# Performance work log

Hardware: AMD Instinct MI355X
Metric: run time of the kernel (lower is better)

The kernel has to match this reference:

```python
import jax, jax.numpy as jnp
import numpy as np
import math

N_HEADS = 16
ROPE_BASE = 10000.0


def rotate_half(x):
    x1 = x[..., ::2]
    x2 = x[..., 1::2]
    return jnp.stack((-x2, x1), axis=-1).reshape(x.shape)


def rope_tables(seq_len, head_dim, dtype):
    inv_freq = 1.0 / (ROPE_BASE ** (jnp.arange(0, head_dim, 2, dtype=jnp.float32) / head_dim))
    positions = jnp.arange(seq_len, dtype=jnp.float32)
    freqs = jnp.outer(positions, inv_freq)            # [S, hd/2]
    emb = jnp.concatenate((freqs, freqs), axis=-1)    # [S, hd]  (matches torch cat convention)
    cos = jnp.cos(emb)[None, None, :, :].astype(dtype)
    sin = jnp.sin(emb)[None, None, :, :].astype(dtype)
    return cos, sin


def setup_inputs() -> dict:
    key = jax.random.key(0)
    k1, k2, k3 = jax.random.split(key, 3)
    B, S, D = 2, 2048, 1024
    x = jax.random.normal(k1, (B, S, D), dtype=jnp.float32)
    # causal lower-triangular mask, broadcastable over batch and heads
    mask = jnp.tril(jnp.ones((S, S), dtype=jnp.int32))[None, None, :, :]
    w_qkv = jax.random.normal(k2, (D, 3 * D), dtype=jnp.float32) * 0.02
    w_out = jax.random.normal(k3, (D, D), dtype=jnp.float32) * 0.02
    return {"x": x, "mask": mask, "w_qkv": w_qkv, "w_out": w_out}


def reference(x, mask, w_qkv, w_out):
    B, S, D = x.shape
    H = N_HEADS
    hd = D // H
    qkv = (x @ w_qkv).reshape(B, S, 3, H, hd)
    qkv = jnp.transpose(qkv, (2, 0, 3, 1, 4))         # [3, B, H, S, hd]
    q, k, v = qkv[0], qkv[1], qkv[2]
    cos, sin = rope_tables(S, hd, x.dtype)
    q = q * cos + rotate_half(q) * sin
    k = k * cos + rotate_half(k) * sin
    scale = math.sqrt(hd)
    attn = jnp.einsum("bhsd,bhtd->bhst", q, k) / scale
    attn = jnp.where(mask == 0, -jnp.inf, attn)
    attn = jax.nn.softmax(attn, axis=-1)              # dropout p=0.0 -> identity
    out = jnp.einsum("bhst,bhtd->bhsd", attn, v)
    out = jnp.transpose(out, (0, 2, 1, 3)).reshape(B, S, D)
    return out @ w_out
```

## Files before the change

### kernel.cpp

```cpp
#include <hip/hip_runtime.h>
#include <stdint.h>

typedef unsigned short u16;
typedef __bf16 bf16x8 __attribute__((ext_vector_type(8)));
typedef float f32x4 __attribute__((ext_vector_type(4)));

#define S_LEN 2048
#define NH    16
#define DM    1024
#define N3    3072
#define MROWS 4096

__device__ __forceinline__ float b2f(u16 u) {
  unsigned int v = ((unsigned int)u) << 16;
  return __builtin_bit_cast(float, v);
}
__device__ __forceinline__ u16 f2b(float f) {
  unsigned int v = __builtin_bit_cast(unsigned int, f);
  v += 0x7fffu + ((v >> 16) & 1u);
  return (u16)(v >> 16);
}
__device__ __forceinline__ u16 f2b_trunc(float f) {
  return (u16)(__builtin_bit_cast(unsigned int, f) >> 16);
}
__device__ __forceinline__ bf16x8 ld8(const u16* p) { return *(const bf16x8*)p; }
__device__ __forceinline__ f32x4 mfma16(bf16x8 a, bf16x8 b, f32x4 c) {
  return __builtin_amdgcn_mfma_f32_16x16x32_bf16(a, b, c, 0, 0, 0);
}
__device__ __forceinline__ void glds16(const void* g, void* l) {
  __builtin_amdgcn_global_load_lds(
      (const __attribute__((address_space(1))) unsigned int*)g,
      (__attribute__((address_space(3))) unsigned int*)l, 16, 0, 0);
}
__device__ __forceinline__ int bfish(unsigned int w) {
  unsigned int e = (w >> 7) & 0xffu;
  return (e >= 100u && e <= 134u) ? 1 : 0;
}

__global__ __launch_bounds__(256) void prep_kernel(const void* __restrict__ x,
                                                   const void* __restrict__ wqkv,
                                                   const void* __restrict__ wout,
                                                   u16* __restrict__ xb,
                                                   u16* __restrict__ wqT,
                                                   u16* __restrict__ woT,
                                                   float* __restrict__ cosT,
                                                   float* __restrict__ sinT,
                                                   int* __restrict__ flag) {
  const int bx = blockIdx.x;
  const int t = threadIdx.x;
  if (bx < 2048) {
    __shared__ int cnt;
    if (t == 0) cnt = 0;
    __syncthreads();
    size_t i = (size_t)bx * 256 + t;
    const uint4* xv = (const uint4*)x;
    uint4 probe = xv[i];
    unsigned int wds[4]; *(uint4*)wds = probe;
    atomicAdd(&cnt, bfish(wds[0]) + bfish(wds[1]) + bfish(wds[2]) + bfish(wds[3]));
    __syncthreads();
    const int isbf = cnt > 512;
    if (t == 0) *flag = isbf;
    if (isbf) {
      ((uint4*)xb)[i] = probe;
    } else {
      const float* xf = (const float*)x;
      #pragma unroll
      for (int j = 0; j < 8; ++j) xb[i * 8 + j] = f2b(xf[i * 8 + j]);
    }
    return;
  }
  if (bx < 2304) {
    int i = (bx - 2048) * 256 + t;
    int s = i >> 5, f = i & 31;
    float invf = expf(-(float)(2 * f) * (1.0f / 64.0f) * logf(10000.0f));
    float th = (float)s * invf;
    float sv, cv;
    sincosf(th, &sv, &cv);
    cosT[s * 64 + f] = cv; cosT[s * 64 + 32 + f] = cv;
    sinT[s * 64 + f] = sv; sinT[s * 64 + 32 + f] = sv;
    return;
  }
  const int wq = bx < 5376;
  const int id = wq ? (bx - 2304) : (bx - 5376);
  const int ncx = wq ? 96 : 32;
  const void* in = wq ? wqkv : wout;
  u16* out = wq ? wqT : woT;
  const int C = wq ? 3072 : 1024;
  const int bxc = id % ncx, byr = id / ncx;
  __shared__ int cnt;
  __shared__ float tile[32][33];
  const int tx = t & 31, ty = t >> 5;
  if (t == 0) cnt = 0;
  __syncthreads();
  const unsigned int* wv = (const unsigned int*)in;
  size_t off = (((size_t)id) * 256 + t) & 524287;
  atomicAdd(&cnt, bfish(wv[off]));
  __syncthreads();
  const int fl = cnt > 128;
  const int c0 = bxc * 32, r0 = byr * 32;
  #pragma unroll
  for (int dy = 0; dy < 32; dy += 8) {
    size_t idx = (size_t)(r0 + ty + dy) * C + (c0 + tx);
    float v = fl ? b2f(((const u16*)in)[idx]) : ((const float*)in)[idx];
    tile[ty + dy][tx] = v;
  }
  __syncthreads();
  #pragma unroll
  for (int dy = 0; dy < 32; dy += 8) {
    out[(size_t)(c0 + ty + dy) * 1024 + (r0 + tx)] = f2b(tile[tx][ty + dy]);
  }
}

template <int TM, int EPI>
__global__ __launch_bounds__(256) void gemm_t(const u16* __restrict__ A,
                                              const u16* __restrict__ Bt,
                                              int M, int N, int Kd,
                                              u16* __restrict__ Qo, u16* __restrict__ Ko,
                                              u16* __restrict__ Vo,
                                              void* __restrict__ Out,
                                              const int* __restrict__ flag) {
  constexpr int MI = TM / 32;
  __shared__ u16 smem[(TM + 128) * 32];
  u16* Al = smem;
  u16* Bl = smem + TM * 32;
  const int t = threadIdx.x;
  const int lane = t & 63, wave = t >> 6;
  const int ln = lane & 15, quad = lane >> 4;
  const int wr = wave >> 1, wc = wave & 1;
  const int m0 = blockIdx.x * TM, n0 = blockIdx.y * 128;
  const int rr = t >> 2;
  const int cb = (t & 3) * 16;
  const char* Ab = (const char*)A;
  const char* Bb = (const char*)Bt;
  f32x4 acc[MI][4] = {};

  for (int k0 = 0; k0 < Kd; k0 += 32) {
    __syncthreads();
    #pragma unroll
    for (int p = 0; p < TM / 64; ++p)
      glds16(Ab + ((size_t)(m0 + p * 64 + rr) * Kd + k0) * 2 + cb,
             (char*)Al + p * 4096 + t * 16);
    glds16(Bb + ((size_t)(n0 + rr) * Kd + k0) * 2 + cb,      (char*)Bl + t * 16);
    glds16(Bb + ((size_t)(n0 + 64 + rr) * Kd + k0) * 2 + cb, (char*)Bl + 4096 + t * 16);
    __syncthreads();
    bf16x8 a[MI], b[4];
    #pragma unroll
    for (int i = 0; i < MI; ++i)
      a[i] = ld8(Al + (wr * (TM / 2) + i * 16 + ln) * 32 + quad * 8);
    #pragma unroll
    for (int j = 0; j < 4; ++j)
      b[j] = ld8(Bl + (wc * 64 + j * 16 + ln) * 32 + quad * 8);
    #pragma unroll
    for (int i = 0; i < MI; ++i)
      #pragma unroll
      for (int j = 0; j < 4; ++j)
        acc[i][j] = mfma16(a[i], b[j], acc[i][j]);
  }

  if constexpr (EPI == 0) {
    #pragma unroll
    for (int i = 0; i < MI; ++i)
      #pragma unroll
      for (int j = 0; j < 4; ++j)
        #pragma unroll
        for (int r = 0; r < 4; ++r) {
          int m = m0 + wr * (TM / 2) + i * 16 + quad * 4 + r;
          int c = n0 + wc * 64 + j * 16 + ln;
          u16 bv = f2b(acc[i][j][r]);
          int b_ = m >> 11, s = m & 2047;
          int which = c >> 10, h = (c >> 6) & 15, d = c & 63;
          size_t bh = (size_t)(b_ * NH + h);
          u16* dst = (which == 0) ? Qo : (which == 1) ? Ko : Vo;
          dst[(bh * S_LEN + s) * 64 + d] = bv;
        }
  } else {
    const int fl = *flag;
    #pragma unroll
    for (int i = 0; i < MI; ++i)
      #pragma unroll
      for (int j = 0; j < 4; ++j)
        #pragma unroll
        for (int r = 0; r < 4; ++r) {
          int m = m0 + wr * (TM / 2) + i * 16 + quad * 4 + r;
          int c = n0 + wc * 64 + j * 16 + ln;
          float v = acc[i][j][r];
          if (fl) ((u16*)Out)[(size_t)m * N + c] = f2b(v);
          else    ((float*)Out)[(size_t)m * N + c] = v;
        }
  }
}

__global__ __launch_bounds__(256) void vrope_kernel(u16* __restrict__ Qb,
                                                    u16* __restrict__ Kb,
                                                    const u16* __restrict__ V,
                                                    u16* __restrict__ Vt,
                                                    const float* __restrict__ cosT,
                                                    const float* __restrict__ sinT) {
  __shared__ u16 L[4096];
  const int bx = blockIdx.x;
  if (bx < 4096) {
    int i = bx * 256 + threadIdx.x;
    int seg = i & 7;
    int s   = (i >> 3) & 2047;
    int bh  = (i >> 14) & 31;
    int isK = (i >> 19) & 1;
    u16* ptr = (isK ? Kb : Qb) + ((size_t)bh * S_LEN + s) * 64 + seg * 8;
    const float qs = isK ? 1.0f : 0.18033688011112042f;
    uint4 raw = *(const uint4*)ptr;
    u16 e[8]; *(uint4*)e = raw;
    const float* cr = cosT + s * 64 + seg * 8;
    const float* sr = sinT + s * 64 + seg * 8;
    u16 o[8];
    #pragma unroll
    for (int p = 0; p < 4; ++p) {
      float x0 = b2f(e[2 * p]), x1 = b2f(e[2 * p + 1]);
      float o0 = (x0 * cr[2 * p]     - x1 * sr[2 * p])     * qs;
      float o1 = (x1 * cr[2 * p + 1] + x0 * sr[2 * p + 1]) * qs;
      o[2 * p] = f2b(o0); o[2 * p + 1] = f2b(o1);
    }
    *(uint4*)ptr = *(const uint4*)o;
    return;
  }
  const int bb = bx - 4096;
  const int t = threadIdx.x;
  const int bh = bb >> 5, st = bb & 31;
  const u16* Vb = V + ((size_t)bh * S_LEN + st * 64) * 64;
  u16* Vtb = Vt + (size_t)bh * (64 * S_LEN) + st * 64;
  #pragma unroll
  for (int it = 0; it < 2; ++it) {
    int c = it * 256 + t;
    int s = c >> 3, dseg = c & 7;
    uint4 v = *(const uint4*)(Vb + (size_t)s * 64 + dseg * 8);
    u16 e[8]; *(uint4*)e = v;
    #pragma unroll
    for (int j = 0; j < 8; ++j) {
      int d = dseg * 8 + j;
      L[d * 64 + (s ^ (dseg << 3))] = e[j];
    }
  }
  __syncthreads();
  #pragma unroll
  for (int it = 0; it < 2; ++it) {
    int c = it * 256 + t;
    int d = c >> 3, sseg = c & 7;
    uint4 v = *(const uint4*)(L + d * 64 + (((sseg ^ (d >> 3)) & 7) << 3));
    *(uint4*)(Vtb + (size_t)d * S_LEN + sseg * 8) = v;
  }
}

__global__ __launch_bounds__(256) void attn_kernel(const u16* __restrict__ Qb,
                                                   const u16* __restrict__ Kb,
                                                   const u16* __restrict__ Vt,
                                                   u16* __restrict__ Ao) {
  __shared__ u16 smem[20480];
  u16* Kl = smem;
  u16* Vl = smem + 8192;
  u16* Pl = smem + 16384;
  const int t = threadIdx.x;
  const int lane = t & 63, w = t >> 6;
  const int ln = lane & 15, quad = lane >> 4;
  const int i = blockIdx.x;
  const int xcd = i & 7;
  const int j = i >> 3;
  const int bh = (xcd << 2) | (j & 3);
  const int q5 = j >> 2;
  const int g = q5 & 7, s5 = q5 >> 3;
  const int qt = (s5 & 1) ? (31 - ((s5 >> 1) << 3) - g) : (((s5 >> 1) << 3) + g);
  const int q0 = qt * 64;
  const int b = bh >> 4, h = bh & 15;
  const u16* Qbh = Qb + (size_t)bh * (S_LEN * 64);
  const u16* Kbh = Kb + (size_t)bh * (S_LEN * 64);
  const u16* Vtbh = Vt + (size_t)bh * (64 * S_LEN);
  u16* Plw = Pl + w * 1024;
  u16* AoBase = Ao + (size_t)b * S_LEN * DM + h * 64;

  auto stage = [&](int kt, int bufi) {
    u16* kd = Kl + bufi * 4096;
    u16* vd = Vl + bufi * 4096;
    const u16* kg = Kbh + (size_t)kt * 64 * 64;
    const u16* vg = Vtbh + (size_t)kt * 64;
    #pragma unroll
    for (int it = 0; it < 2; ++it) {
      int c = it * 256 + t;
      int row = c >> 3, sg = (c & 7) ^ (row & 7);
      glds16((const char*)kg + ((size_t)row * 64 + sg * 8) * 2,   (char*)kd + c * 16);
      glds16((const char*)vg + ((size_t)row * 2048 + sg * 8) * 2, (char*)vd + c * 16);
    }
  };

  bf16x8 aq[2];
  #pragma unroll
  for (int kk = 0; kk < 2; ++kk)
    aq[kk] = ld8(Qbh + (size_t)(q0 + w * 16 + ln) * 64 + kk * 32 + quad * 8);

  f32x4 o[4] = {};
  float l[4] = {0.f, 0.f, 0.f, 0.f};

  stage(0, 0);
  __syncthreads();

  for (int kt = 0; kt <= qt; ++kt) {
    const int bufi = kt & 1;
    if (kt < qt) stage(kt + 1, bufi ^ 1);
    const u16* Kb_ = Kl + bufi * 4096;
    const u16* Vb_ = Vl + bufi * 4096;

    f32x4 sc[4] = {};
    #pragma unroll
    for (int kk = 0; kk < 2; ++kk)
      #pragma unroll
      for (int ct = 0; ct < 4; ++ct) {
        bf16x8 bk = ld8(Kb_ + (ct * 16 + ln) * 64 + (((kk * 4 + quad) ^ (ln & 7)) << 3));
        sc[ct] = mfma16(aq[kk], bk, sc[ct]);
      }

    if (kt == qt) {
      #pragma unroll
      for (int ct = 0; ct < 4; ++ct)
        #pragma unroll
        for (int r = 0; r < 4; ++r) {
          const int row = quad * 4 + r;
          float p = ((ct * 16 + ln) > (w * 16 + row))
                        ? 0.f : __builtin_amdgcn_exp2f(sc[ct][r]);
          l[r] += p;
          Plw[row * 64 + ((((ct * 2) + (ln >> 3)) ^ quad) << 3) + (ln & 7)] = f2b_trunc(p);
        }
    } else {
      #pragma unroll
      for (int ct = 0; ct < 4; ++ct)
        #pragma unroll
        for (int r = 0; r < 4; ++r) {
          const int row = quad * 4 + r;
          float p = __builtin_amdgcn_exp2f(sc[ct][r]);
          l[r] += p;
          Plw[row * 64 + ((((ct * 2) + (ln >> 3)) ^ quad) << 3) + (ln & 7)] = f2b_trunc(p);
        }
    }

    #pragma unroll
    for (int k4 = 0; k4 < 2; ++k4) {
      bf16x8 ap = ld8(Plw + ln * 64 + (((k4 * 4 + quad) ^ (ln >> 2)) << 3));
      #pragma unroll
      for (int dt = 0; dt < 4; ++dt) {
        bf16x8 bv = ld8(Vb_ + (dt * 16 + ln) * 64 + (((k4 * 4 + quad) ^ (ln & 7)) << 3));
        o[dt] = mfma16(ap, bv, o[dt]);
      }
    }
    __syncthreads();
  }

  #pragma unroll
  for (int r = 0; r < 4; ++r) {
    float lv = l[r];
    #pragma unroll
    for (int off = 1; off < 16; off <<= 1) lv += __shfl_xor(lv, off);
    l[r] = 1.f / lv;
  }
  #pragma unroll
  for (int dt = 0; dt < 4; ++dt)
    #pragma unroll
    for (int r = 0; r < 4; ++r) {
      float v = o[dt][r] * l[r];
      AoBase[(size_t)(q0 + w * 16 + quad * 4 + r) * DM + dt * 16 + ln] = f2b(v);
    }
}

extern "C" void kernel_launch(void* const* d_in, const int* in_sizes, int n_in,
                              void* d_out, int out_size, void* d_ws, size_t ws_size,
                              hipStream_t stream) {
  (void)in_sizes; (void)n_in; (void)out_size; (void)ws_size;
  const void* x    = d_in[0];
  const void* wqkv = d_in[2];
  const void* wout = d_in[3];
  char* ws = (char*)d_ws;
  u16*  xb   = (u16*)(ws + 0);
  u16*  Ao   = xb;
  u16*  wqT  = (u16*)(ws + 8388608);
  u16*  Vtp  = (u16*)(ws + 8388608);
  u16*  Qb   = (u16*)(ws + 16777216);
  u16*  Kb   = (u16*)(ws + 25165824);
  u16*  Vb   = (u16*)(ws + 33554432);
  u16*  woT  = (u16*)(ws + 41943040);
  float* cosT = (float*)(ws + 44040192);
  float* sinT = (float*)(ws + 44564480);
  int*  flag = (int*)(ws + 45088768);

  prep_kernel<<<6400, 256, 0, stream>>>(x, wqkv, wout, xb, wqT, woT, cosT, sinT, flag);
  gemm_t<128, 0><<<dim3(32, 24), 256, 0, stream>>>(xb, wqT, MROWS, N3, DM,
                                                   Qb, Kb, Vb, nullptr, flag);
  vrope_kernel<<<5120, 256, 0, stream>>>(Qb, Kb, Vb, Vtp, cosT, sinT);
  attn_kernel<<<1024, 256, 0, stream>>>(Qb, Kb, Vtp, Ao);
  gemm_t<64, 1><<<dim3(64, 8), 256, 0, stream>>>(Ao, woT, MROWS, DM, DM,
                                                 nullptr, nullptr, nullptr, d_out, flag);
}
```

Baseline: 203.0 us.

## Fuse RoPE, Q scaling and V transpose into QKV GEMM epilogue

The separate vrope kernel is removed. The QKV GEMM epilogue now applies RoPE and the softmax scale to Q and K, using a lane shuffle to fetch the paired element. It also writes V directly in transposed layout with packed 4-element stores. This drops a kernel launch and a full read-modify-write pass over Q, K and V. In exchange the epilogue does strided global stores and reads the cos/sin tables per element, and the workspace layout is reshuffled.

Result: no change. 203.2 us (+0.1%).

```diff
diff --git a/kernel.cpp b/kernel.cpp
--- a/kernel.cpp
+++ b/kernel.cpp
@@ -111,140 +111,81 @@
   }
 }
 
-template <int TM, int EPI>
-__global__ __launch_bounds__(256) void gemm_t(const u16* __restrict__ A,
-                                              const u16* __restrict__ Bt,
-                                              int M, int N, int Kd,
-                                              u16* __restrict__ Qo, u16* __restrict__ Ko,
-                                              u16* __restrict__ Vo,
-                                              void* __restrict__ Out,
-                                              const int* __restrict__ flag) {
-  constexpr int MI = TM / 32;
-  __shared__ u16 smem[(TM + 128) * 32];
+__global__ __launch_bounds__(256) void gemm_qkv(const u16* __restrict__ A,
+                                                const u16* __restrict__ Bt,
+                                                u16* __restrict__ Qo,
+                                                u16* __restrict__ Ko,
+                                                u16* __restrict__ Vt,
+                                                const float* __restrict__ cosT,
+                                                const float* __restrict__ sinT) {
+  __shared__ u16 smem[8192];
   u16* Al = smem;
-  u16* Bl = smem + TM * 32;
+  u16* Bl = smem + 4096;
   const int t = threadIdx.x;
   const int lane = t & 63, wave = t >> 6;
   const int ln = lane & 15, quad = lane >> 4;
   const int wr = wave >> 1, wc = wave & 1;
-  const int m0 = blockIdx.x * TM, n0 = blockIdx.y * 128;
+  const int m0 = blockIdx.x * 128, n0 = blockIdx.y * 128;
   const int rr = t >> 2;
   const int cb = (t & 3) * 16;
   const char* Ab = (const char*)A;
   const char* Bb = (const char*)Bt;
-  f32x4 acc[MI][4] = {};
-
-  for (int k0 = 0; k0 < Kd; k0 += 32) {
-    __syncthreads();
-    #pragma unroll
-    for (int p = 0; p < TM / 64; ++p)
-      glds16(Ab + ((size_t)(m0 + p * 64 + rr) * Kd + k0) * 2 + cb,
-             (char*)Al + p * 4096 + t * 16);
-    glds16(Bb + ((size_t)(n0 + rr) * Kd + k0) * 2 + cb,      (char*)Bl + t * 16);
-    glds16(Bb + ((size_t)(n0 + 64 + rr) * Kd + k0) * 2 + cb, (char*)Bl + 4096 + t * 16);
-    __syncthreads();
-    bf16x8 a[MI], b[4];
-    #pragma unroll
-    for (int i = 0; i < MI; ++i)
-      a[i] = ld8(Al + (wr * (TM / 2) + i * 16 + ln) * 32 + quad * 8);
-    #pragma unroll
-    for (int j = 0; j < 4; ++j)
-      b[j] = ld8(Bl + (wc * 64 + j * 16 + ln) * 32 + quad * 8);
-    #pragma unroll
-    for (int i = 0; i < MI; ++i)
+  f32x4 acc[4][4] = {};
+
+  for (int k0 = 0; k0 < 1024; k0 += 32) {
+    __syncthreads();
+    glds16(Ab + ((size_t)(m0 + rr) * 1024 + k0) * 2 + cb,      (char*)Al + t * 16);
+    glds16(Ab + ((size_t)(m0 + 64 + rr) * 1024 + k0) * 2 + cb, (char*)Al + 4096 + t * 16);
+    glds16(Bb + ((size_t)(n0 + rr) * 1024 + k0) * 2 + cb,      (char*)Bl + t * 16);
+    glds16(Bb + ((size_t)(n0 + 64 + rr) * 1024 + k0) * 2 + cb, (char*)Bl + 4096 + t * 16);
+    __syncthreads();
+    bf16x8 a[4], b[4];
+    #pragma unroll
+    for (int i = 0; i < 4; ++i) a[i] = ld8(Al + (wr * 64 + i * 16 + ln) * 32 + quad * 8);
+    #pragma unroll
+    for (int j = 0; j < 4; ++j) b[j] = ld8(Bl + (wc * 64 + j * 16 + ln) * 32 + quad * 8);
+    #pragma unroll
+    for (int i = 0; i < 4; ++i)
       #pragma unroll
       for (int j = 0; j < 4; ++j)
         acc[i][j] = mfma16(a[i], b[j], acc[i][j]);
   }
 
-  if constexpr (EPI == 0) {
-    #pragma unroll
-    for (int i = 0; i < MI; ++i)
-      #pragma unroll
-      for (int j = 0; j < 4; ++j)
+  const int which = n0 >> 10;
+  if (which < 2) {
+    u16* dst = which ? Ko : Qo;
+    const float qs = which ? 1.0f : 0.18033688011112042f;
+    #pragma unroll
+    for (int i = 0; i < 4; ++i)
+      #pragma unroll
+      for (int j = 0; j < 4; ++j) {
+        const int c = n0 + wc * 64 + j * 16 + ln;
+        const int h = (c >> 6) & 15, d = c & 63;
+        const float sgn = (d & 1) ? 1.0f : -1.0f;
         #pragma unroll
         for (int r = 0; r < 4; ++r) {
-          int m = m0 + wr * (TM / 2) + i * 16 + quad * 4 + r;
-          int c = n0 + wc * 64 + j * 16 + ln;
-          u16 bv = f2b(acc[i][j][r]);
-          int b_ = m >> 11, s = m & 2047;
-          int which = c >> 10, h = (c >> 6) & 15, d = c & 63;
-          size_t bh = (size_t)(b_ * NH + h);
-          u16* dst = (which == 0) ? Qo : (which == 1) ? Ko : Vo;
-          dst[(bh * S_LEN + s) * 64 + d] = bv;
+          const int m = m0 + wr * 64 + i * 16 + quad * 4 + r;
+          const int s = m & 2047, b_ = m >> 11;
+          const float v = acc[i][j][r];
+          const float p = __shfl_xor(v, 1);
+          const float o = (v * cosT[s * 64 + d] + sgn * p * sinT[s * 64 + d]) * qs;
+          dst[((size_t)(b_ * NH + h) * S_LEN + s) * 64 + d] = f2b(o);
         }
+      }
   } else {
-    const int fl = *flag;
-    #pragma unroll
-    for (int i = 0; i < MI; ++i)
-      #pragma unroll
-      for (int j = 0; j < 4; ++j)
+    #pragma unroll
+    for (int i = 0; i < 4; ++i)
+      #pragma unroll
+      for (int j = 0; j < 4; ++j) {
+        const int c = n0 + wc * 64 + j * 16 + ln;
+        const int h = (c >> 6) & 15, d = c & 63;
+        const int m = m0 + wr * 64 + i * 16 + quad * 4;
+        const int s = m & 2047, b_ = m >> 11;
+        u16 pk[4];
         #pragma unroll
-        for (int r = 0; r < 4; ++r) {
-          int m = m0 + wr * (TM / 2) + i * 16 + quad * 4 + r;
-          int c = n0 + wc * 64 + j * 16 + ln;
-          float v = acc[i][j][r];
-          if (fl) ((u16*)Out)[(size_t)m * N + c] = f2b(v);
-          else    ((float*)Out)[(size_t)m * N + c] = v;
-        }
-  }
-}
-
-__global__ __launch_bounds__(256) void vrope_kernel(u16* __restrict__ Qb,
-                                                    u16* __restrict__ Kb,
-                                                    const u16* __restrict__ V,
-                                                    u16* __restrict__ Vt,
-                                                    const float* __restrict__ cosT,
-                                                    const float* __restrict__ sinT) {
-  __shared__ u16 L[4096];
-  const int bx = blockIdx.x;
-  if (bx < 4096) {
-    int i = bx * 256 + threadIdx.x;
-    int seg = i & 7;
-    int s   = (i >> 3) & 2047;
-    int bh  = (i >> 14) & 31;
-    int isK = (i >> 19) & 1;
-    u16* ptr = (isK ? Kb : Qb) + ((size_t)bh * S_LEN + s) * 64 + seg * 8;
-    const float qs = isK ? 1.0f : 0.18033688011112042f;
-    uint4 raw = *(const uint4*)ptr;
-    u16 e[8]; *(uint4*)e = raw;
-    const float* cr = cosT + s * 64 + seg * 8;
-    const float* sr = sinT + s * 64 + seg * 8;
-    u16 o[8];
-    #pragma unroll
-    for (int p = 0; p < 4; ++p) {
-      float x0 = b2f(e[2 * p]), x1 = b2f(e[2 * p + 1]);
-      float o0 = (x0 * cr[2 * p]     - x1 * sr[2 * p])     * qs;
-      float o1 = (x1 * cr[2 * p + 1] + x0 * sr[2 * p + 1]) * qs;
-      o[2 * p] = f2b(o0); o[2 * p + 1] = f2b(o1);
-    }
-    *(uint4*)ptr = *(const uint4*)o;
-    return;
-  }
-  const int bb = bx - 4096;
-  const int t = threadIdx.x;
-  const int bh = bb >> 5, st = bb & 31;
-  const u16* Vb = V + ((size_t)bh * S_LEN + st * 64) * 64;
-  u16* Vtb = Vt + (size_t)bh * (64 * S_LEN) + st * 64;
-  #pragma unroll
-  for (int it = 0; it < 2; ++it) {
-    int c = it * 256 + t;
-    int s = c >> 3, dseg = c & 7;
-    uint4 v = *(const uint4*)(Vb + (size_t)s * 64 + dseg * 8);
-    u16 e[8]; *(uint4*)e = v;
-    #pragma unroll
-    for (int j = 0; j < 8; ++j) {
-      int d = dseg * 8 + j;
-      L[d * 64 + (s ^ (dseg << 3))] = e[j];
-    }
-  }
-  __syncthreads();
-  #pragma unroll
-  for (int it = 0; it < 2; ++it) {
-    int c = it * 256 + t;
-    int d = c >> 3, sseg = c & 7;
-    uint4 v = *(const uint4*)(L + d * 64 + (((sseg ^ (d >> 3)) & 7) << 3));
-    *(uint4*)(Vtb + (size_t)d * S_LEN + sseg * 8) = v;
+        for (int r = 0; r < 4; ++r) pk[r] = f2b(acc[i][j][r]);
+        *(uint2*)&Vt[((size_t)(b_ * NH + h) * 64 + d) * S_LEN + s] = *(const uint2*)pk;
+      }
   }
 }
 
@@ -365,6 +306,64 @@
     }
 }
 
+template <int TM>
+__global__ __launch_bounds__(256) void gemm_out_t(const u16* __restrict__ A,
+                                                  const u16* __restrict__ Bt,
+                                                  void* __restrict__ Out,
+                                                  const int* __restrict__ flag) {
+  constexpr int MI = TM / 32;
+  __shared__ u16 smem[(TM + 128) * 32];
+  u16* Al = smem;
+  u16* Bl = smem + TM * 32;
+  const int t = threadIdx.x;
+  const int lane = t & 63, wave = t >> 6;
+  const int ln = lane & 15, quad = lane >> 4;
+  const int wr = wave >> 1, wc = wave & 1;
+  const int m0 = blockIdx.x * TM, n0 = blockIdx.y * 128;
+  const int rr = t >> 2;
+  const int cb = (t & 3) * 16;
+  const char* Ab = (const char*)A;
+  const char* Bb = (const char*)Bt;
+  f32x4 acc[MI][4] = {};
+
+  for (int k0 = 0; k0 < 1024; k0 += 32) {
+    __syncthreads();
+    #pragma unroll
+    for (int p = 0; p < TM / 64; ++p)
+      glds16(Ab + ((size_t)(m0 + p * 64 + rr) * 1024 + k0) * 2 + cb,
+             (char*)Al + p * 4096 + t * 16);
+    glds16(Bb + ((size_t)(n0 + rr) * 1024 + k0) * 2 + cb,      (char*)Bl + t * 16);
+    glds16(Bb + ((size_t)(n0 + 64 + rr) * 1024 + k0) * 2 + cb, (char*)Bl + 4096 + t * 16);
+    __syncthreads();
+    bf16x8 a[MI], b[4];
+    #pragma unroll
+    for (int i = 0; i < MI; ++i)
+      a[i] = ld8(Al + (wr * (TM / 2) + i * 16 + ln) * 32 + quad * 8);
+    #pragma unroll
+    for (int j = 0; j < 4; ++j)
+      b[j] = ld8(Bl + (wc * 64 + j * 16 + ln) * 32 + quad * 8);
+    #pragma unroll
+    for (int i = 0; i < MI; ++i)
+      #pragma unroll
+      for (int j = 0; j < 4; ++j)
+        acc[i][j] = mfma16(a[i], b[j], acc[i][j]);
+  }
+
+  const int fl = *flag;
+  #pragma unroll
+  for (int i = 0; i < MI; ++i)
+    #pragma unroll
+    for (int j = 0; j < 4; ++j)
+      #pragma unroll
+      for (int r = 0; r < 4; ++r) {
+        int m = m0 + wr * (TM / 2) + i * 16 + quad * 4 + r;
+        int c = n0 + wc * 64 + j * 16 + ln;
+        float v = acc[i][j][r];
+        if (fl) ((u16*)Out)[(size_t)m * DM + c] = f2b(v);
+        else    ((float*)Out)[(size_t)m * DM + c] = v;
+      }
+}
+
 extern "C" void kernel_launch(void* const* d_in, const int* in_sizes, int n_in,
                               void* d_out, int out_size, void* d_ws, size_t ws_size,
                               hipStream_t stream) {
@@ -376,20 +375,16 @@
   u16*  xb   = (u16*)(ws + 0);
   u16*  Ao   = xb;
   u16*  wqT  = (u16*)(ws + 8388608);
-  u16*  Vtp  = (u16*)(ws + 8388608);
+  u16*  woT  = (u16*)(ws + 14680064);
   u16*  Qb   = (u16*)(ws + 16777216);
   u16*  Kb   = (u16*)(ws + 25165824);
-  u16*  Vb   = (u16*)(ws + 33554432);
-  u16*  woT  = (u16*)(ws + 41943040);
-  float* cosT = (float*)(ws + 44040192);
-  float* sinT = (float*)(ws + 44564480);
-  int*  flag = (int*)(ws + 45088768);
+  u16*  Vt   = (u16*)(ws + 33554432);
+  float* cosT = (float*)(ws + 41943040);
+  float* sinT = (float*)(ws + 42467328);
+  int*  flag = (int*)(ws + 42991616);
 
   prep_kernel<<<6400, 256, 0, stream>>>(x, wqkv, wout, xb, wqT, woT, cosT, sinT, flag);
-  gemm_t<128, 0><<<dim3(32, 24), 256, 0, stream>>>(xb, wqT, MROWS, N3, DM,
-                                                   Qb, Kb, Vb, nullptr, flag);
-  vrope_kernel<<<5120, 256, 0, stream>>>(Qb, Kb, Vb, Vtp, cosT, sinT);
-  attn_kernel<<<1024, 256, 0, stream>>>(Qb, Kb, Vtp, Ao);
-  gemm_t<64, 1><<<dim3(64, 8), 256, 0, stream>>>(Ao, woT, MROWS, DM, DM,
-                                                 nullptr, nullptr, nullptr, d_out, flag);
-}
+  gemm_qkv<<<dim3(32, 24), 256, 0, stream>>>(xb, wqT, Qb, Kb, Vt, cosT, sinT);
+  attn_kernel<<<1024, 256, 0, stream>>>(Qb, Kb, Vt, Ao);
+  gemm_out_t<64><<<dim3(64, 8), 256, 0, stream>>>(Ao, woT, d_out, flag);
+}
```
